# Kernel tuning notes

Hardware: AMD Instinct MI355X
Metric: run time of the kernel (lower is better)

Reference implementation:

```python
import jax, jax.numpy as jnp
import numpy as np

VOXEL_SIZE = np.array([0.16, 0.16, 4.0], dtype=np.float32)
PC_MIN = np.array([0.0, -39.68, -3.0], dtype=np.float32)
BN_EPS_VFE = 1e-3
BN_EPS_OUT = 1e-5


def _batchnorm(h, gamma, beta, axes, eps):
    # training-mode batchnorm: biased batch statistics over `axes`
    mean = jnp.mean(h, axis=axes, keepdims=True)
    var = jnp.mean(jnp.square(h - mean), axis=axes, keepdims=True)
    return gamma * (h - mean) * jax.lax.rsqrt(var + eps) + beta


def _vfe_layer(x, num_points, W, gamma, beta):
    # x: (B, V, P, Cin); W: (Cout//2, Cin) -> concat output has Cout channels
    B, V, P, _ = x.shape
    h = jnp.einsum('bvpc,oc->bvpo', x, W)               # linear, no bias (use_norm)
    h = _batchnorm(h, gamma, beta, axes=(0, 1, 2), eps=BN_EPS_VFE)
    h = jax.nn.relu(h)
    mx = jnp.max(h, axis=2, keepdims=True)              # masked-max surrogate (orig maxes padded rows too)
    comb = jnp.concatenate([h, jnp.broadcast_to(mx, h.shape)], axis=-1)
    mask = (jnp.arange(P)[None, None, :, None] < num_points[:, :, None, None]).astype(h.dtype)
    return comb * mask


def setup_inputs() -> dict:
    key = jax.random.key(0)
    ks = jax.random.split(key, 12)
    B, V, P, Cin = 2, 16000, 32, 4
    voxels = jax.random.normal(ks[0], (B, V, P, Cin), dtype=jnp.float32)
    voxel_coords = jax.random.randint(ks[1], (B, V, 4), 0, 400).astype(jnp.int32)
    voxel_num_points = jax.random.randint(ks[2], (B, V), 0, P).astype(jnp.int32)
    s = 0.1
    return {
        'voxels': voxels,
        'voxel_coords': voxel_coords,
        'voxel_num_points': voxel_num_points,
        'W1': jax.random.normal(ks[3], (16, 8), dtype=jnp.float32) * s,
        'gamma1': jnp.ones((16,), jnp.float32), 'beta1': jnp.zeros((16,), jnp.float32),
        'W2': jax.random.normal(ks[4], (32, 32), dtype=jnp.float32) * s,
        'gamma2': jnp.ones((32,), jnp.float32), 'beta2': jnp.zeros((32,), jnp.float32),
        'Wf': jax.random.normal(ks[5], (64, 64), dtype=jnp.float32) * s,
        'gammaf': jnp.ones((64,), jnp.float32), 'betaf': jnp.zeros((64,), jnp.float32),
    }


def reference(voxels, voxel_coords, voxel_num_points,
              W1, gamma1, beta1, W2, gamma2, beta2, Wf, gammaf, betaf):
    pts_xyz = voxels[..., :3]                            # (B,V,P,3)
    pts_feat = voxels[..., 3:]                           # (B,V,P,1)
    # voxel centers from [z,y,x] indices -> [x,y,z]
    idx = voxel_coords[:, :, 1:4].astype(jnp.float32)[..., ::-1]  # (B,V,3) xyz
    centers = (idx + 0.5) * jnp.asarray(VOXEL_SIZE) + jnp.asarray(PC_MIN)
    rel = pts_xyz - centers[:, :, None, :]
    height = pts_xyz[..., 2:3]
    feats = jnp.concatenate([pts_xyz, rel, pts_feat, height], axis=-1)  # (B,V,P,8)

    h = _vfe_layer(feats, voxel_num_points, W1, gamma1, beta1)   # (B,V,P,32)
    h = _vfe_layer(h, voxel_num_points, W2, gamma2, beta2)       # (B,V,P,64)

    vfeat = jnp.max(h, axis=2)                                   # (B,V,64) max-pool over points
    vfeat = jnp.einsum('bvc,oc->bvo', vfeat, Wf)                 # linear, no bias
    vfeat = _batchnorm(vfeat, gammaf, betaf, axes=(0, 1), eps=BN_EPS_OUT)
    return vfeat
```

## Files before the change

kernel.cpp:

```cpp
#include <hip/hip_runtime.h>

#define NVOX 32000
#define NPTS 1024000
#define NBLK 1000
#define NWAV 4000
#define VPW  8
#define BIGF 1e30f

typedef __attribute__((ext_vector_type(8)))  short bf8v;
typedef __attribute__((ext_vector_type(16))) float f16x;

__device__ __forceinline__ void split2(float x, short* hi, short* lo) {
    const unsigned u = __float_as_uint(x);
    *hi = (short)(u >> 16);
    const float r = x - __uint_as_float(u & 0xFFFF0000u);
    *lo = (short)(__float_as_uint(r) >> 16);
}
__device__ __forceinline__ float rdlane(float v, int l) {
    return __int_as_float(__builtin_amdgcn_readlane(__float_as_int(v), l));
}

#define OF_W1S  480
#define OF_C1S  (480+128)
#define OF_A2C2 (480+144)
#define OF_AFCF (480+208)

__global__ void kz(double* __restrict__ s) {
    if (threadIdx.x < 236) s[threadIdx.x] = 0.0;
}

__global__ __launch_bounds__(256) void k1(const float* __restrict__ vox,
                                          const int* __restrict__ coords,
                                          double* __restrict__ sF) {
    float S[8], U[36];
#pragma unroll
    for (int a = 0; a < 8; a++) S[a] = 0.f;
#pragma unroll
    for (int a = 0; a < 36; a++) U[a] = 0.f;
    const int stride = gridDim.x * blockDim.x;
    for (int i = blockIdx.x * blockDim.x + threadIdx.x; i < NPTS; i += stride) {
        const int vx = i >> 5;
        const float4 q = reinterpret_cast<const float4*>(vox)[i];
        const int4 c4 = reinterpret_cast<const int4*>(coords)[vx];
        const float cx = ((float)c4.w + 0.5f) * 0.16f;
        const float cy = ((float)c4.z + 0.5f) * 0.16f - 39.68f;
        const float cz = ((float)c4.y + 0.5f) * 4.0f  - 3.0f;
        const float f[8] = {q.x, q.y, q.z, q.x - cx, q.y - cy, q.z - cz, q.w, q.z};
        int u = 0;
#pragma unroll
        for (int a = 0; a < 8; a++) {
            S[a] += f[a];
#pragma unroll
            for (int b = a; b < 8; b++) { U[u] = fmaf(f[a], f[b], U[u]); u++; }
        }
    }
    __shared__ float red[4][44];
    const int lane = threadIdx.x & 63, wv = threadIdx.x >> 6;
#pragma unroll
    for (int t = 0; t < 44; t++) {
        float s = (t < 8) ? S[t] : U[t - 8];
#pragma unroll
        for (int m = 1; m < 64; m <<= 1) s += __shfl_xor(s, m);
        if (lane == 0) red[wv][t] = s;
    }
    __syncthreads();
    if (threadIdx.x < 44) {
        const float t = red[0][threadIdx.x] + red[1][threadIdx.x] +
                        red[2][threadIdx.x] + red[3][threadIdx.x];
        atomicAdd(&sF[threadIdx.x], (double)t);
    }
}

__global__ __launch_bounds__(128) void kr1(const double* __restrict__ sF,
                                           const float* __restrict__ W1,
                                           const float* __restrict__ g1,
                                           const float* __restrict__ b1,
                                           float* __restrict__ w1s,
                                           float* __restrict__ c1s) {
    __shared__ float a1f[16];
    const int t = threadIdx.x;
    if (t < 16) {
        double w[8];
#pragma unroll
        for (int c = 0; c < 8; c++) w[c] = (double)W1[t * 8 + c];
        double mu = 0.0;
#pragma unroll
        for (int c = 0; c < 8; c++) mu += w[c] * sF[c];
        double sq = 0.0;
        int u = 8;
        for (int a = 0; a < 8; a++)
            for (int b = a; b < 8; b++) {
                const double F = sF[u++];
                sq += (a == b ? 1.0 : 2.0) * w[a] * w[b] * F;
            }
        const double m = mu * (1.0 / NPTS);
        const double v = sq * (1.0 / NPTS) - m * m;
        const float inv = rsqrtf((float)v + 1e-3f);
        const float aa = g1[t] * inv;
        a1f[t] = aa;
        c1s[t] = b1[t] - (float)m * aa;
    }
    __syncthreads();
    w1s[t] = a1f[t >> 3] * W1[t];
}

__global__ __launch_bounds__(256, 4) void k2(const float* __restrict__ vox,
                                             const int* __restrict__ coords,
                                             const int* __restrict__ nump,
                                             const float* __restrict__ w1s,
                                             const float* __restrict__ c1s,
                                             const float* __restrict__ W2,
                                             const float* __restrict__ g2,
                                             double* __restrict__ s2,
                                             float* __restrict__ outp) {
    const int l = threadIdx.x & 63, wv = threadIdx.x >> 6;
    const int p = l & 31, hf = l >> 5;

    bf8v b1h, b1l, b2h, b2l;
#pragma unroll
    for (int i = 0; i < 8; i++) {
        short h_, l_;
        split2(W2[p * 32 + 8 * hf + i], &h_, &l_);       b1h[i] = h_; b1l[i] = l_;
        split2(W2[p * 32 + 16 + 8 * hf + i], &h_, &l_);  b2h[i] = h_; b2l[i] = l_;
    }
    const bool useMax = (g2[p] >= 0.f);

    float tsum = 0.f, tsq = 0.f;
    const int gw = blockIdx.x * 4 + wv;
#pragma unroll 1
    for (int v = 0; v < VPW; ++v) {
        const int vx = gw + v * NWAV;
        const int4 c4 = reinterpret_cast<const int4*>(coords)[vx];
        const int np = nump[vx];
        const float4 q = reinterpret_cast<const float4*>(vox)[(vx << 5) + p];
        const float cx = ((float)c4.w + 0.5f) * 0.16f;
        const float cy = ((float)c4.z + 0.5f) * 0.16f - 39.68f;
        const float cz = ((float)c4.y + 0.5f) * 4.0f  - 3.0f;
        const float f[8] = {q.x, q.y, q.z, q.x - cx, q.y - cy, q.z - cz, q.w, q.z};
        float mine[8], mx[8];
#pragma unroll
        for (int i = 0; i < 8; i++) {
            float s0 = c1s[i], s1v = c1s[8 + i];
#pragma unroll
            for (int c = 0; c < 8; c++) {
                s0 = fmaf(f[c], w1s[i * 8 + c], s0);
                s1v = fmaf(f[c], w1s[(8 + i) * 8 + c], s1v);
            }
            mine[i] = fmaxf(hf ? s1v : s0, 0.f);
        }
#pragma unroll
        for (int i = 0; i < 8; i++) {
            float m = mine[i];
            m = fmaxf(m, __shfl_xor(m, 1));
            m = fmaxf(m, __shfl_xor(m, 2));
            m = fmaxf(m, __shfl_xor(m, 4));
            m = fmaxf(m, __shfl_xor(m, 8));
            m = fmaxf(m, __shfl_xor(m, 16));
            mx[i] = m;
        }
        const float mk = (p < np) ? 1.f : 0.f;
        bf8v a1h, a1l, a2h, a2l;
#pragma unroll
        for (int i = 0; i < 8; i++) {
            short h_, l_;
            split2(mk * mine[i], &h_, &l_);  a1h[i] = h_; a1l[i] = l_;
            split2(mk * mx[i], &h_, &l_);    a2h[i] = h_; a2l[i] = l_;
        }
        f16x d;
#pragma unroll
        for (int r = 0; r < 16; r++) d[r] = 0.f;
        d = __builtin_amdgcn_mfma_f32_32x32x16_bf16(a1h, b1h, d, 0, 0, 0);
        d = __builtin_amdgcn_mfma_f32_32x32x16_bf16(a1l, b1h, d, 0, 0, 0);
        d = __builtin_amdgcn_mfma_f32_32x32x16_bf16(a1h, b1l, d, 0, 0, 0);
        d = __builtin_amdgcn_mfma_f32_32x32x16_bf16(a2h, b2h, d, 0, 0, 0);
        d = __builtin_amdgcn_mfma_f32_32x32x16_bf16(a2l, b2h, d, 0, 0, 0);
        d = __builtin_amdgcn_mfma_f32_32x32x16_bf16(a2h, b2l, d, 0, 0, 0);

        float mmx = -BIGF, mmn = BIGF, fmx = -BIGF, fmn = BIGF;
#pragma unroll
        for (int r = 0; r < 16; r++) {
            const int row = (r & 3) + 8 * (r >> 2) + 4 * hf;
            const float x = d[r];
            tsum += x;
            tsq = fmaf(x, x, tsq);
            fmx = fmaxf(fmx, x);
            fmn = fminf(fmn, x);
            const bool in = row < np;
            mmx = fmaxf(mmx, in ? x : -BIGF);
            mmn = fminf(mmn, in ? x : BIGF);
        }
        mmx = fmaxf(mmx, __shfl_xor(mmx, 32));
        mmn = fminf(mmn, __shfl_xor(mmn, 32));
        fmx = fmaxf(fmx, __shfl_xor(fmx, 32));
        fmn = fminf(fmn, __shfl_xor(fmn, 32));
        const float e = hf ? (useMax ? fmx : fmn) : (useMax ? mmx : mmn);
        outp[(vx << 6) + l] = e;
    }

    tsum += __shfl_xor(tsum, 32);
    tsq  += __shfl_xor(tsq, 32);
    __shared__ float red[4][64];
    if (l < 32) { red[wv][l] = tsum; red[wv][32 + l] = tsq; }
    __syncthreads();
    if (threadIdx.x < 64) {
        const float t = red[0][threadIdx.x] + red[1][threadIdx.x] +
                        red[2][threadIdx.x] + red[3][threadIdx.x];
        atomicAdd(&s2[threadIdx.x], (double)t);
    }
}

__global__ __launch_bounds__(64) void kr2(const double* __restrict__ s2,
                                          const float* __restrict__ g2,
                                          const float* __restrict__ b2,
                                          float* __restrict__ a2c2) {
    const int t = threadIdx.x;
    if (t < 32) {
        const double m = s2[t] * (1.0 / NPTS);
        const double v = s2[32 + t] * (1.0 / NPTS) - m * m;
        const float inv = rsqrtf((float)v + 1e-3f);
        const float aa = g2[t] * inv;
        a2c2[t] = aa;
        a2c2[32 + t] = b2[t] - (float)m * aa;
    }
}

__global__ __launch_bounds__(256, 3) void k3(const int* __restrict__ nump,
                                             const float* __restrict__ a2c2,
                                             const float* __restrict__ Wf,
                                             double* __restrict__ sfin,
                                             float* __restrict__ outp) {
    const int l = threadIdx.x & 63, wv = threadIdx.x >> 6;
    const int p = l & 31;

    const float a2v = a2c2[p];
    const float c2v = a2c2[32 + p];

    float wfr[64];
#pragma unroll
    for (int j = 0; j < 16; j++) {
        const float4 w4 = reinterpret_cast<const float4*>(Wf)[l * 16 + j];
        wfr[4 * j] = w4.x; wfr[4 * j + 1] = w4.y; wfr[4 * j + 2] = w4.z; wfr[4 * j + 3] = w4.w;
    }

    __shared__ float red[4][128];

    float ts = 0.f, tq = 0.f;
    const int gw = blockIdx.x * 4 + wv;
#pragma unroll 1
    for (int v = 0; v < VPW; ++v) {
        const int vx = gw + v * NWAV;
        const int np = nump[vx];
        const float x = outp[(vx << 6) + l];
        const float h2 = fmaxf(fmaf(a2v, x, c2v), 0.f);
        const float bc = (np > 0) ? h2 : 0.f;

        float o0 = 0.f, o1 = 0.f, o2 = 0.f, o3 = 0.f;
#pragma unroll
        for (int c = 0; c < 64; c += 4) {
            o0 = fmaf(rdlane(bc, c),     wfr[c],     o0);
            o1 = fmaf(rdlane(bc, c + 1), wfr[c + 1], o1);
            o2 = fmaf(rdlane(bc, c + 2), wfr[c + 2], o2);
            o3 = fmaf(rdlane(bc, c + 3), wfr[c + 3], o3);
        }
        const float out = (o0 + o1) + (o2 + o3);
        outp[(vx << 6) + l] = out;
        ts += out;
        tq = fmaf(out, out, tq);
    }

    red[wv][l] = ts;
    red[wv][64 + l] = tq;
    __syncthreads();
    if (threadIdx.x < 128) {
        const float t = red[0][threadIdx.x] + red[1][threadIdx.x] +
                        red[2][threadIdx.x] + red[3][threadIdx.x];
        atomicAdd(&sfin[threadIdx.x], (double)t);
    }
}

__global__ __launch_bounds__(64) void kr3(const double* __restrict__ sfin,
                                          const float* __restrict__ gf,
                                          const float* __restrict__ bfv,
                                          float* __restrict__ afcf) {
    const int t = threadIdx.x;
    const double m = sfin[t] * (1.0 / NVOX);
    const double v = sfin[64 + t] * (1.0 / NVOX) - m * m;
    const float inv = rsqrtf((float)v + 1e-5f);
    const float aa = gf[t] * inv;
    afcf[t] = aa;
    afcf[64 + t] = bfv[t] - (float)m * aa;
}

__global__ __launch_bounds__(256) void k4(float* __restrict__ outp,
                                          const float* __restrict__ afcf) {
    const int tid = blockIdx.x * blockDim.x + threadIdx.x;
    const int o = (tid * 4) & 63;
    float4 v = reinterpret_cast<float4*>(outp)[tid];
    v.x = fmaf(afcf[o],     v.x, afcf[64 + o]);
    v.y = fmaf(afcf[o + 1], v.y, afcf[65 + o]);
    v.z = fmaf(afcf[o + 2], v.z, afcf[66 + o]);
    v.w = fmaf(afcf[o + 3], v.w, afcf[67 + o]);
    reinterpret_cast<float4*>(outp)[tid] = v;
}

extern "C" void kernel_launch(void* const* d_in, const int* in_sizes, int n_in,
                              void* d_out, int out_size, void* d_ws, size_t ws_size,
                              hipStream_t stream) {
    const float* vox    = (const float*)d_in[0];
    const int*   coords = (const int*)d_in[1];
    const int*   nump   = (const int*)d_in[2];
    const float* W1     = (const float*)d_in[3];
    const float* g1     = (const float*)d_in[4];
    const float* b1     = (const float*)d_in[5];
    const float* W2     = (const float*)d_in[6];
    const float* g2     = (const float*)d_in[7];
    const float* b2     = (const float*)d_in[8];
    const float* Wf     = (const float*)d_in[9];
    const float* gf     = (const float*)d_in[10];
    const float* bfv    = (const float*)d_in[11];
    float* out = (float*)d_out;

    double* sF   = (double*)d_ws;
    double* s2   = sF + 44;
    double* sfin = sF + 108;
    float*  wsf  = (float*)d_ws;
    float*  W1S  = wsf + OF_W1S;
    float*  C1S  = wsf + OF_C1S;
    float*  A2C2 = wsf + OF_A2C2;
    float*  AFCF = wsf + OF_AFCF;

    kz<<<1, 256, 0, stream>>>(sF);
    k1<<<1024, 256, 0, stream>>>(vox, coords, sF);
    kr1<<<1, 128, 0, stream>>>(sF, W1, g1, b1, W1S, C1S);
    k2<<<NBLK, 256, 0, stream>>>(vox, coords, nump, W1S, C1S, W2, g2, s2, out);
    kr2<<<1, 64, 0, stream>>>(s2, g2, b2, A2C2);
    k3<<<NBLK, 256, 0, stream>>>(nump, A2C2, Wf, sfin, out);
    kr3<<<1, 64, 0, stream>>>(sfin, gf, bfv, AFCF);
    k4<<<2000, 256, 0, stream>>>(out, AFCF);
}
```

Before: 216.0 us.

## Fold BN finalize kernels into consumers, sign-flip min/max, double grid sizes

Removes the tiny kr2 and kr3 launches by recomputing the batchnorm scale and shift inside k3 and k4, which cuts two serialized kernel launches. The k2 epilogue uses a sign-bit XOR so that a single max reduction stands in for the separate max and min paths, which halves the reduction and shuffle work. Grids for k1, k2 and k3 are doubled with fewer voxels per wave, and the occupancy hints are raised to 8 for k2 and 4 for k3. This risks register spills at the higher occupancy, adds redundant per-thread finalize work and doubles the number of atomic adds.

```diff
diff --git a/kernel.cpp b/kernel.cpp
--- a/kernel.cpp
+++ b/kernel.cpp
@@ -2,9 +2,9 @@
 
 #define NVOX 32000
 #define NPTS 1024000
-#define NBLK 1000
-#define NWAV 4000
-#define VPW  8
+#define KBLK 2000
+#define KWAV 8000
+#define KVPW 4
 #define BIGF 1e30f
 
 typedef __attribute__((ext_vector_type(8)))  short bf8v;
@@ -22,8 +22,6 @@
 
 #define OF_W1S  480
 #define OF_C1S  (480+128)
-#define OF_A2C2 (480+144)
-#define OF_AFCF (480+208)
 
 __global__ void kz(double* __restrict__ s) {
     if (threadIdx.x < 236) s[threadIdx.x] = 0.0;
@@ -104,7 +102,7 @@
     w1s[t] = a1f[t >> 3] * W1[t];
 }
 
-__global__ __launch_bounds__(256, 4) void k2(const float* __restrict__ vox,
+__global__ __launch_bounds__(256, 8) void k2(const float* __restrict__ vox,
                                              const int* __restrict__ coords,
                                              const int* __restrict__ nump,
                                              const float* __restrict__ w1s,
@@ -123,13 +121,13 @@
         split2(W2[p * 32 + 8 * hf + i], &h_, &l_);       b1h[i] = h_; b1l[i] = l_;
         split2(W2[p * 32 + 16 + 8 * hf + i], &h_, &l_);  b2h[i] = h_; b2l[i] = l_;
     }
-    const bool useMax = (g2[p] >= 0.f);
+    const unsigned sbit = (g2[p] >= 0.f) ? 0u : 0x80000000u;
 
     float tsum = 0.f, tsq = 0.f;
     const int gw = blockIdx.x * 4 + wv;
 #pragma unroll 1
-    for (int v = 0; v < VPW; ++v) {
-        const int vx = gw + v * NWAV;
+    for (int v = 0; v < KVPW; ++v) {
+        const int vx = gw + v * KWAV;
         const int4 c4 = reinterpret_cast<const int4*>(coords)[vx];
         const int np = nump[vx];
         const float4 q = reinterpret_cast<const float4*>(vox)[(vx << 5) + p];
@@ -176,24 +174,20 @@
         d = __builtin_amdgcn_mfma_f32_32x32x16_bf16(a2l, b2h, d, 0, 0, 0);
         d = __builtin_amdgcn_mfma_f32_32x32x16_bf16(a2h, b2l, d, 0, 0, 0);
 
-        float mmx = -BIGF, mmn = BIGF, fmx = -BIGF, fmn = BIGF;
+        float fx = -BIGF, mxv = -BIGF;
 #pragma unroll
         for (int r = 0; r < 16; r++) {
             const int row = (r & 3) + 8 * (r >> 2) + 4 * hf;
             const float x = d[r];
             tsum += x;
             tsq = fmaf(x, x, tsq);
-            fmx = fmaxf(fmx, x);
-            fmn = fminf(fmn, x);
-            const bool in = row < np;
-            mmx = fmaxf(mmx, in ? x : -BIGF);
-            mmn = fminf(mmn, in ? x : BIGF);
-        }
-        mmx = fmaxf(mmx, __shfl_xor(mmx, 32));
-        mmn = fminf(mmn, __shfl_xor(mmn, 32));
-        fmx = fmaxf(fmx, __shfl_xor(fmx, 32));
-        fmn = fminf(fmn, __shfl_xor(fmn, 32));
-        const float e = hf ? (useMax ? fmx : fmn) : (useMax ? mmx : mmn);
+            const float xs = __uint_as_float(__float_as_uint(x) ^ sbit);
+            fx = fmaxf(fx, xs);
+            mxv = fmaxf(mxv, (row < np) ? xs : -BIGF);
+        }
+        fx  = fmaxf(fx,  __shfl_xor(fx, 32));
+        mxv = fmaxf(mxv, __shfl_xor(mxv, 32));
+        const float e = __uint_as_float(__float_as_uint(hf ? fx : mxv) ^ sbit);
         outp[(vx << 6) + l] = e;
     }
 
@@ -209,31 +203,20 @@
     }
 }
 
-__global__ __launch_bounds__(64) void kr2(const double* __restrict__ s2,
-                                          const float* __restrict__ g2,
-                                          const float* __restrict__ b2,
-                                          float* __restrict__ a2c2) {
-    const int t = threadIdx.x;
-    if (t < 32) {
-        const double m = s2[t] * (1.0 / NPTS);
-        const double v = s2[32 + t] * (1.0 / NPTS) - m * m;
-        const float inv = rsqrtf((float)v + 1e-3f);
-        const float aa = g2[t] * inv;
-        a2c2[t] = aa;
-        a2c2[32 + t] = b2[t] - (float)m * aa;
-    }
-}
-
-__global__ __launch_bounds__(256, 3) void k3(const int* __restrict__ nump,
-                                             const float* __restrict__ a2c2,
+__global__ __launch_bounds__(256, 4) void k3(const int* __restrict__ nump,
+                                             const double* __restrict__ s2,
+                                             const float* __restrict__ g2,
+                                             const float* __restrict__ b2,
                                              const float* __restrict__ Wf,
                                              double* __restrict__ sfin,
                                              float* __restrict__ outp) {
     const int l = threadIdx.x & 63, wv = threadIdx.x >> 6;
     const int p = l & 31;
 
-    const float a2v = a2c2[p];
-    const float c2v = a2c2[32 + p];
+    const double m2 = s2[p] * (1.0 / NPTS);
+    const double v2 = s2[32 + p] * (1.0 / NPTS) - m2 * m2;
+    const float a2v = g2[p] * rsqrtf((float)v2 + 1e-3f);
+    const float c2v = b2[p] - (float)m2 * a2v;
 
     float wfr[64];
 #pragma unroll
@@ -247,8 +230,8 @@
     float ts = 0.f, tq = 0.f;
     const int gw = blockIdx.x * 4 + wv;
 #pragma unroll 1
-    for (int v = 0; v < VPW; ++v) {
-        const int vx = gw + v * NWAV;
+    for (int v = 0; v < KVPW; ++v) {
+        const int vx = gw + v * KWAV;
         const int np = nump[vx];
         const float x = outp[(vx << 6) + l];
         const float h2 = fmaxf(fmaf(a2v, x, c2v), 0.f);
@@ -278,28 +261,27 @@
     }
 }
 
-__global__ __launch_bounds__(64) void kr3(const double* __restrict__ sfin,
+__global__ __launch_bounds__(256) void k4(float* __restrict__ outp,
+                                          const double* __restrict__ sfin,
                                           const float* __restrict__ gf,
-                                          const float* __restrict__ bfv,
-                                          float* __restrict__ afcf) {
-    const int t = threadIdx.x;
-    const double m = sfin[t] * (1.0 / NVOX);
-    const double v = sfin[64 + t] * (1.0 / NVOX) - m * m;
-    const float inv = rsqrtf((float)v + 1e-5f);
-    const float aa = gf[t] * inv;
-    afcf[t] = aa;
-    afcf[64 + t] = bfv[t] - (float)m * aa;
-}
-
-__global__ __launch_bounds__(256) void k4(float* __restrict__ outp,
-                                          const float* __restrict__ afcf) {
+                                          const float* __restrict__ bfv) {
+    __shared__ float af[64], cf[64];
+    if (threadIdx.x < 64) {
+        const int t = threadIdx.x;
+        const double m = sfin[t] * (1.0 / NVOX);
+        const double v = sfin[64 + t] * (1.0 / NVOX) - m * m;
+        const float aa = gf[t] * rsqrtf((float)v + 1e-5f);
+        af[t] = aa;
+        cf[t] = bfv[t] - (float)m * aa;
+    }
+    __syncthreads();
     const int tid = blockIdx.x * blockDim.x + threadIdx.x;
     const int o = (tid * 4) & 63;
     float4 v = reinterpret_cast<float4*>(outp)[tid];
-    v.x = fmaf(afcf[o],     v.x, afcf[64 + o]);
-    v.y = fmaf(afcf[o + 1], v.y, afcf[65 + o]);
-    v.z = fmaf(afcf[o + 2], v.z, afcf[66 + o]);
-    v.w = fmaf(afcf[o + 3], v.w, afcf[67 + o]);
+    v.x = fmaf(af[o],     v.x, cf[o]);
+    v.y = fmaf(af[o + 1], v.y, cf[o + 1]);
+    v.z = fmaf(af[o + 2], v.z, cf[o + 2]);
+    v.w = fmaf(af[o + 3], v.w, cf[o + 3]);
     reinterpret_cast<float4*>(outp)[tid] = v;
 }
 
@@ -326,15 +308,11 @@
     float*  wsf  = (float*)d_ws;
     float*  W1S  = wsf + OF_W1S;
     float*  C1S  = wsf + OF_C1S;
-    float*  A2C2 = wsf + OF_A2C2;
-    float*  AFCF = wsf + OF_AFCF;
 
     kz<<<1, 256, 0, stream>>>(sF);
-    k1<<<1024, 256, 0, stream>>>(vox, coords, sF);
+    k1<<<2048, 256, 0, stream>>>(vox, coords, sF);
     kr1<<<1, 128, 0, stream>>>(sF, W1, g1, b1, W1S, C1S);
-    k2<<<NBLK, 256, 0, stream>>>(vox, coords, nump, W1S, C1S, W2, g2, s2, out);
-    kr2<<<1, 64, 0, stream>>>(s2, g2, b2, A2C2);
-    k3<<<NBLK, 256, 0, stream>>>(nump, A2C2, Wf, sfin, out);
-    kr3<<<1, 64, 0, stream>>>(sfin, gf, bfv, AFCF);
-    k4<<<2000, 256, 0, stream>>>(out, AFCF);
-}
+    k2<<<KBLK, 256, 0, stream>>>(vox, coords, nump, W1S, C1S, W2, g2, s2, out);
+    k3<<<KBLK, 256, 0, stream>>>(nump, s2, g2, b2, Wf, sfin, out);
+    k4<<<2000, 256, 0, stream>>>(out, sfin, gf, bfv);
+}
```

After: 314.0 us. +45.4%, slower.
